# Kernel tuning notes

Measured on AMD Instinct MI355X. Metric: run time of the kernel, lower is better.

Reference implementation:

```python
import jax, jax.numpy as jnp
import numpy as np

N = 100000   # nodes
E = 1000000  # edges
H = 64       # hidden_channels
L = 3        # num_layers
B = 256      # graphs in batch
VOCAB = 100  # embedding table size


def _gru(m, h, wih, whh, bih, bhh):
    # torch.nn.GRUCell semantics, gate order r, z, n
    gi = m @ wih.T + bih            # [N, 3H]
    gh = h @ whh.T + bhh            # [N, 3H]
    ir, iz, inn = jnp.split(gi, 3, axis=-1)
    hr, hz, hn = jnp.split(gh, 3, axis=-1)
    r = jax.nn.sigmoid(ir + hr)
    z = jax.nn.sigmoid(iz + hz)
    n = jnp.tanh(inn + r * hn)
    return (1.0 - z) * n + z * h


def setup_inputs() -> dict:
    key = jax.random.key(0)
    ks = jax.random.split(key, 20)
    s = 1.0 / np.sqrt(H)
    inp = {
        "x": jax.random.randint(ks[0], (N, 1), 0, VOCAB),
        "edge_index": jax.random.randint(ks[1], (2, E), 0, N),
        "edge_attr": jax.random.uniform(ks[2], (E, 1), dtype=jnp.float32),
        "batch": jnp.sort(jax.random.randint(ks[3], (N,), 0, B)),
        "node_emb": jax.random.normal(ks[4], (VOCAB, H), jnp.float32),
        "edge_W": jax.random.normal(ks[5], (H, 1), jnp.float32) * s,
        "edge_b": jnp.zeros((H,), jnp.float32),
        "ggc_W": jax.random.normal(ks[6], (L, H, H), jnp.float32) * s,
        "gru_wih": jax.random.normal(ks[7], (L, 3 * H, H), jnp.float32) * s,
        "gru_whh": jax.random.normal(ks[8], (L, 3 * H, H), jnp.float32) * s,
        "gru_bih": jnp.zeros((L, 3 * H), jnp.float32),
        "gru_bhh": jnp.zeros((L, 3 * H), jnp.float32),
        "fc1_W": jax.random.normal(ks[9], (H // 2, H), jnp.float32) * s,
        "fc1_b": jnp.zeros((H // 2,), jnp.float32),
        "fc2_W": jax.random.normal(ks[10], (H // 4, H // 2), jnp.float32) * (1.0 / np.sqrt(H // 2)),
        "fc2_b": jnp.zeros((H // 4,), jnp.float32),
        "fc3_W": jax.random.normal(ks[11], (1, H // 4), jnp.float32) * (1.0 / np.sqrt(H // 4)),
        "fc3_b": jnp.zeros((1,), jnp.float32),
    }
    return inp


def reference(x, edge_index, edge_attr, batch, node_emb, edge_W, edge_b,
              ggc_W, gru_wih, gru_whh, gru_bih, gru_bhh,
              fc1_W, fc1_b, fc2_W, fc2_b, fc3_W, fc3_b):
    h = node_emb[x[:, 0]]                       # [N, H] node embedding
    _e = edge_attr @ edge_W.T + edge_b          # computed in original, unused by convs
    src, dst = edge_index[0], edge_index[1]
    for l in range(L):
        m = h @ ggc_W[l]                        # per-node linear transform
        agg = jax.ops.segment_sum(m[src], dst, num_segments=N)  # scatter-add to dst
        h = _gru(agg, h, gru_wih[l], gru_whh[l], gru_bih[l], gru_bhh[l])
        h = jax.nn.relu(h)                      # dropout = identity in eval
    sums = jax.ops.segment_sum(h, batch, num_segments=B)
    counts = jax.ops.segment_sum(jnp.ones((N, 1), h.dtype), batch, num_segments=B)
    pooled = sums / jnp.maximum(counts, 1.0)    # global_mean_pool
    y = jax.nn.relu(pooled @ fc1_W.T + fc1_b)
    y = jax.nn.relu(y @ fc2_W.T + fc2_b)
    y = y @ fc3_W.T + fc3_b
    return y[:, 0]                              # squeeze(-1) -> [B]
```

## Files before the change

kernel.cpp:

```cpp
#include <hip/hip_runtime.h>
#include <cstdint>

using h8v = __attribute__((ext_vector_type(8))) _Float16;
using h4v = __attribute__((ext_vector_type(4))) _Float16;
using f4v = __attribute__((ext_vector_type(4))) float;

__device__ __forceinline__ float sigmoidf_(float x) {
  return 1.0f / (1.0f + __expf(-x));
}
__device__ __forceinline__ float tanhf_(float x) {
  return 2.0f / (1.0f + __expf(-2.0f * x)) - 1.0f;
}

#define BN 256
#define BCAP 4096
#define NBMAX 1024

__global__ __launch_bounds__(256) void k_embed(const int* __restrict__ x,
                                               const float* __restrict__ emb,
                                               _Float16* __restrict__ h16, int N) {
  int idx = blockIdx.x * 256 + threadIdx.x;
  if (idx >= N * 64) return;
  int i = idx >> 6, j = idx & 63;
  h16[idx] = (_Float16)emb[x[i] * 64 + j];
}

__global__ __launch_bounds__(256) void k_hist(const int* __restrict__ dst,
                                              int* __restrict__ hist, int E) {
  __shared__ int lh[NBMAX];
  for (int i = threadIdx.x; i < NBMAX; i += 256) lh[i] = 0;
  __syncthreads();
  for (int e = blockIdx.x * 256 + threadIdx.x; e < E; e += gridDim.x * 256)
    atomicAdd(&lh[dst[e] >> 8], 1);
  __syncthreads();
  for (int i = threadIdx.x; i < NBMAX; i += 256)
    if (lh[i]) atomicAdd(&hist[i], lh[i]);
}

__global__ __launch_bounds__(1024) void k_bscan(const int* __restrict__ hist,
                                                int* __restrict__ bbase,
                                                int* __restrict__ rowp,
                                                int nb, int N, int E) {
  __shared__ int sc[NBMAX];
  int t = threadIdx.x;
  int v = (t < nb) ? hist[t] : 0;
  sc[t] = v;
  __syncthreads();
  for (int off = 1; off < NBMAX; off <<= 1) {
    int xx = (t >= off) ? sc[t - off] : 0;
    __syncthreads();
    sc[t] += xx;
    __syncthreads();
  }
  if (t <= nb) bbase[t] = sc[t] - v;
  if (t == 0) rowp[N] = E;
}

#define EPB 4096
__global__ __launch_bounds__(256) void k_scatter(const int* __restrict__ src,
                                                 const int* __restrict__ dst,
                                                 const int* __restrict__ bbase,
                                                 int* __restrict__ cursor,
                                                 unsigned* __restrict__ ebuf,
                                                 int E, int nb) {
  __shared__ int lh[NBMAX];
  __shared__ int lbase[NBMAX];
  for (int i = threadIdx.x; i < NBMAX; i += 256) lh[i] = 0;
  __syncthreads();
  const int e0 = blockIdx.x * EPB;
  const int e1 = min(e0 + EPB, E);
  for (int e = e0 + threadIdx.x; e < e1; e += 256) atomicAdd(&lh[dst[e] >> 8], 1);
  __syncthreads();
  for (int i = threadIdx.x; i < nb; i += 256) {
    int c = lh[i];
    lbase[i] = c ? (bbase[i] + atomicAdd(&cursor[i], c)) : 0;
    lh[i] = 0;
  }
  __syncthreads();
  for (int e = e0 + threadIdx.x; e < e1; e += 256) {
    int d = dst[e];
    int b = d >> 8;
    int off = atomicAdd(&lh[b], 1);
    ebuf[lbase[b] + off] = ((unsigned)(d & 255) << 20) | (unsigned)src[e];
  }
}

__global__ __launch_bounds__(256) void k_csr(const unsigned* __restrict__ ebuf,
                                             const int* __restrict__ bbase,
                                             int* __restrict__ rowp,
                                             int* __restrict__ ssrc, int N) {
  __shared__ unsigned se[BCAP];
  __shared__ int ss[BCAP];
  __shared__ int cnt[BN], excl[BN], sc[BN];
  const int b = blockIdx.x;
  const int t = threadIdx.x;
  const int nbeg = b * BN;
  const int ebeg = bbase[b];
  int ne = bbase[b + 1] - ebeg;
  if (ne > BCAP) ne = BCAP;
  for (int i = t; i < ne; i += 256) se[i] = ebuf[ebeg + i];
  cnt[t] = 0;
  __syncthreads();
  for (int i = t; i < ne; i += 256) atomicAdd(&cnt[se[i] >> 20], 1);
  __syncthreads();
  int v = cnt[t];
  sc[t] = v;
  __syncthreads();
  for (int off = 1; off < BN; off <<= 1) {
    int xx = (t >= off) ? sc[t - off] : 0;
    __syncthreads();
    sc[t] += xx;
    __syncthreads();
  }
  excl[t] = sc[t] - v;
  if (nbeg + t < N) rowp[nbeg + t] = ebeg + excl[t];
  cnt[t] = 0;
  __syncthreads();
  for (int i = t; i < ne; i += 256) {
    unsigned e = se[i];
    int dL = e >> 20;
    int off = atomicAdd(&cnt[dL], 1);
    ss[excl[dL] + off] = (int)(e & 0xFFFFF);
  }
  __syncthreads();
  for (int i = t; i < ne; i += 256) ssrc[ebeg + i] = ss[i];
}

__global__ __launch_bounds__(256) void k_wpack3(const float* __restrict__ wih_all,
                                                const float* __restrict__ ggc_all,
                                                const float* __restrict__ whh_all,
                                                _Float16* __restrict__ Bp) {
  int l = blockIdx.x >> 4;
  int tid = (blockIdx.x & 15) * 256 + threadIdx.x;
  const float* wih = wih_all + (size_t)l * 192 * 64;
  const float* ggc = ggc_all + (size_t)l * 64 * 64;
  const float* whh = whh_all + (size_t)l * 192 * 64;
  int lane = tid & 63;
  int t = (tid >> 6) & 3;
  int wg = tid >> 8;
  int g = wg & 3, w = wg >> 2;
  int j = 16 * w + (lane & 15);
  int kbase = t * 32 + (lane >> 4) * 8;
  _Float16 hv[8];
#pragma unroll
  for (int i = 0; i < 8; ++i) {
    int k = kbase + i;
    float v = 0.0f;
    if (k < 64) {
      if (g < 3) {
        const float* a = wih + (size_t)(g * 64 + j) * 64;
        const float* bp = ggc + (size_t)k * 64;
        float s = 0.0f;
#pragma unroll
        for (int m = 0; m < 64; ++m) s += a[m] * bp[m];
        v = s;
      }
    } else {
      if (g != 2) {
        int row = (g == 3 ? 2 : g) * 64 + j;
        v = whh[(size_t)row * 64 + (k - 64)];
      }
    }
    hv[i] = (_Float16)v;
  }
  _Float16* o = Bp + (size_t)l * 32768 + (size_t)tid * 8;
#pragma unroll
  for (int i = 0; i < 8; ++i) o[i] = hv[i];
}

__device__ __forceinline__ h8v f32lds_to_h8(const float* __restrict__ p) {
  f4v x0 = *(const f4v*)p;
  f4v x1 = *(const f4v*)(p + 4);
  h8v r;
#pragma unroll
  for (int i = 0; i < 4; ++i) {
    r[i] = (_Float16)x0[i];
    r[4 + i] = (_Float16)x1[i];
  }
  return r;
}

#define FSTRIDE 68
#define HSTRIDE 72

__global__ __launch_bounds__(256, 4) void k_gfu(const _Float16* __restrict__ hin16,
                                                _Float16* __restrict__ hout16,
                                                const int* __restrict__ rowp,
                                                const int* __restrict__ ssrc,
                                                const _Float16* __restrict__ Bp,
                                                const float* __restrict__ bih,
                                                const float* __restrict__ bhh,
                                                const int* __restrict__ batch,
                                                float* __restrict__ psum,
                                                float* __restrict__ pcnt,
                                                int N, int nTiles, int last) {
  __shared__ float aggLds[16 * FSTRIDE];
  __shared__ _Float16 hLds[16 * HSTRIDE];
  __shared__ _Float16 oLds[16 * HSTRIDE];
  const int lane = threadIdx.x & 63;
  const int w = threadIdx.x >> 6;
  const int r15 = lane & 15;
  const int kg8 = (lane >> 4) * 8;
  const int jj = w * 16 + r15;

  const float b_r = bih[jj] + bhh[jj];
  const float b_z = bih[64 + jj] + bhh[64 + jj];
  const float b_i = bih[128 + jj];
  const float b_h = bhh[128 + jj];

  h8v b0[4], b1[4], b2[2], b3[2];
#pragma unroll
  for (int t = 0; t < 4; ++t) {
    b0[t] = *(const h8v*)(Bp + ((size_t)((w * 4 + 0) * 4 + t) * 64 + lane) * 8);
    b1[t] = *(const h8v*)(Bp + ((size_t)((w * 4 + 1) * 4 + t) * 64 + lane) * 8);
  }
#pragma unroll
  for (int t = 0; t < 2; ++t) {
    b2[t] = *(const h8v*)(Bp + ((size_t)((w * 4 + 2) * 4 + t) * 64 + lane) * 8);
    b3[t] = *(const h8v*)(Bp + ((size_t)((w * 4 + 3) * 4 + (2 + t)) * 64 + lane) * 8);
  }

  for (int tile = blockIdx.x; tile < nTiles; tile += gridDim.x) {
    const int n0 = tile * 16;
    __syncthreads();
    {
      const int g = lane >> 4;
      const int node = 4 * w + g;
      const int n = n0 + node;
      const int nc = min(n, N - 1);
      h4v hv = *(const h4v*)(hin16 + (size_t)nc * 64 + 4 * r15);
      f4v a0 = {0, 0, 0, 0}, a1 = {0, 0, 0, 0}, a2 = {0, 0, 0, 0}, a3 = {0, 0, 0, 0};
      if (n < N) {
        int e = rowp[n];
        const int end = rowp[n + 1];
        for (; e + 8 <= end; e += 8) {
          int s0 = ssrc[e], s1 = ssrc[e + 1], s2 = ssrc[e + 2], s3 = ssrc[e + 3];
          int s4 = ssrc[e + 4], s5 = ssrc[e + 5], s6 = ssrc[e + 6], s7 = ssrc[e + 7];
          h4v v0 = *(const h4v*)(hin16 + (size_t)s0 * 64 + 4 * r15);
          h4v v1 = *(const h4v*)(hin16 + (size_t)s1 * 64 + 4 * r15);
          h4v v2 = *(const h4v*)(hin16 + (size_t)s2 * 64 + 4 * r15);
          h4v v3 = *(const h4v*)(hin16 + (size_t)s3 * 64 + 4 * r15);
          h4v v4 = *(const h4v*)(hin16 + (size_t)s4 * 64 + 4 * r15);
          h4v v5 = *(const h4v*)(hin16 + (size_t)s5 * 64 + 4 * r15);
          h4v v6 = *(const h4v*)(hin16 + (size_t)s6 * 64 + 4 * r15);
          h4v v7 = *(const h4v*)(hin16 + (size_t)s7 * 64 + 4 * r15);
          a0 += __builtin_convertvector(v0, f4v);
          a1 += __builtin_convertvector(v1, f4v);
          a2 += __builtin_convertvector(v2, f4v);
          a3 += __builtin_convertvector(v3, f4v);
          a0 += __builtin_convertvector(v4, f4v);
          a1 += __builtin_convertvector(v5, f4v);
          a2 += __builtin_convertvector(v6, f4v);
          a3 += __builtin_convertvector(v7, f4v);
        }
        if (e + 4 <= end) {
          int s0 = ssrc[e], s1 = ssrc[e + 1], s2 = ssrc[e + 2], s3 = ssrc[e + 3];
          a0 += __builtin_convertvector(*(const h4v*)(hin16 + (size_t)s0 * 64 + 4 * r15), f4v);
          a1 += __builtin_convertvector(*(const h4v*)(hin16 + (size_t)s1 * 64 + 4 * r15), f4v);
          a2 += __builtin_convertvector(*(const h4v*)(hin16 + (size_t)s2 * 64 + 4 * r15), f4v);
          a3 += __builtin_convertvector(*(const h4v*)(hin16 + (size_t)s3 * 64 + 4 * r15), f4v);
          e += 4;
        }
        if (e + 2 <= end) {
          int s0 = ssrc[e], s1 = ssrc[e + 1];
          a0 += __builtin_convertvector(*(const h4v*)(hin16 + (size_t)s0 * 64 + 4 * r15), f4v);
          a1 += __builtin_convertvector(*(const h4v*)(hin16 + (size_t)s1 * 64 + 4 * r15), f4v);
          e += 2;
        }
        if (e < end) {
          int s0 = ssrc[e];
          a2 += __builtin_convertvector(*(const h4v*)(hin16 + (size_t)s0 * 64 + 4 * r15), f4v);
        }
      }
      a0 += a1; a2 += a3; a0 += a2;
      *(f4v*)(aggLds + node * FSTRIDE + 4 * r15) = a0;
      *(h4v*)(hLds + node * HSTRIDE + 4 * r15) = hv;
    }
    __syncthreads();

    h8v ah[4];
#pragma unroll
    for (int t = 0; t < 2; ++t)
      ah[t] = f32lds_to_h8(aggLds + r15 * FSTRIDE + t * 32 + kg8);
#pragma unroll
    for (int t = 0; t < 2; ++t)
      ah[2 + t] = *(const h8v*)(hLds + r15 * HSTRIDE + t * 32 + kg8);

    f4v acc0 = {0, 0, 0, 0}, acc1 = {0, 0, 0, 0}, acc2 = {0, 0, 0, 0}, acc3 = {0, 0, 0, 0};
#pragma unroll
    for (int t = 0; t < 4; ++t) {
      acc0 = __builtin_amdgcn_mfma_f32_16x16x32_f16(ah[t], b0[t], acc0, 0, 0, 0);
      acc1 = __builtin_amdgcn_mfma_f32_16x16x32_f16(ah[t], b1[t], acc1, 0, 0, 0);
    }
    acc2 = __builtin_amdgcn_mfma_f32_16x16x32_f16(ah[0], b2[0], acc2, 0, 0, 0);
    acc2 = __builtin_amdgcn_mfma_f32_16x16x32_f16(ah[1], b2[1], acc2, 0, 0, 0);
    acc3 = __builtin_amdgcn_mfma_f32_16x16x32_f16(ah[2], b3[0], acc3, 0, 0, 0);
    acc3 = __builtin_amdgcn_mfma_f32_16x16x32_f16(ah[3], b3[1], acc3, 0, 0, 0);

    const int rb = (lane >> 4) * 4;
#pragma unroll
    for (int q = 0; q < 4; ++q) {
      int row = rb + q;
      float hold = (float)hLds[row * HSTRIDE + jj];
      float r = sigmoidf_(acc0[q] + b_r);
      float z = sigmoidf_(acc1[q] + b_z);
      float nv = tanhf_(acc2[q] + b_i + r * (acc3[q] + b_h));
      float o = (1.0f - z) * nv + z * hold;
      oLds[row * HSTRIDE + jj] = (_Float16)fmaxf(o, 0.0f);
    }
    __syncthreads();

    if (!last) {
      const int node = threadIdx.x >> 4;
      const int ci = (threadIdx.x & 15) * 4;
      const int n = n0 + node;
      if (n < N) {
        h4v o = *(const h4v*)(oLds + node * HSTRIDE + ci);
        *(h4v*)(hout16 + (size_t)n * 64 + ci) = o;
      }
    } else {
      if (threadIdx.x < 64) {
        int curb = batch[n0];
        float acc = 0.0f, ca = 0.0f;
#pragma unroll 1
        for (int i = 0; i < 16; ++i) {
          int n = n0 + i;
          if (n >= N) break;
          int b = batch[n];
          if (b != curb) {
            atomicAdd(&psum[curb * 64 + lane], acc);
            if (lane == 0) atomicAdd(&pcnt[curb], ca);
            acc = 0.0f; ca = 0.0f; curb = b;
          }
          acc += (float)oLds[i * HSTRIDE + lane];
          ca += 1.0f;
        }
        atomicAdd(&psum[curb * 64 + lane], acc);
        if (lane == 0) atomicAdd(&pcnt[curb], ca);
      }
    }
  }
}

__global__ __launch_bounds__(64) void k_head(const float* __restrict__ psum,
                                             const float* __restrict__ pcnt,
                                             const float* __restrict__ fc1W,
                                             const float* __restrict__ fc1b,
                                             const float* __restrict__ fc2W,
                                             const float* __restrict__ fc2b,
                                             const float* __restrict__ fc3W,
                                             const float* __restrict__ fc3b,
                                             float* __restrict__ out) {
  int b = blockIdx.x;
  int j = threadIdx.x;
  float c = fmaxf(pcnt[b], 1.0f);
  float p = psum[b * 64 + j] / c;
  int j1 = j & 31;
  float y1 = fc1b[j1];
#pragma unroll
  for (int k = 0; k < 64; ++k) y1 += fc1W[j1 * 64 + k] * __shfl(p, k, 64);
  y1 = fmaxf(y1, 0.0f);
  int j2 = j & 15;
  float y2 = fc2b[j2];
#pragma unroll
  for (int k = 0; k < 32; ++k) y2 += fc2W[j2 * 32 + k] * __shfl(y1, k, 64);
  y2 = fmaxf(y2, 0.0f);
  float y = 0.0f;
#pragma unroll
  for (int k = 0; k < 16; ++k) y += fc3W[k] * __shfl(y2, k, 64);
  if (j == 0) out[b] = y + fc3b[0];
}

extern "C" void kernel_launch(void* const* d_in, const int* in_sizes, int n_in,
                              void* d_out, int out_size, void* d_ws, size_t ws_size,
                              hipStream_t stream) {
  const int N = in_sizes[0];
  const int E = in_sizes[1] / 2;
  const int B = out_size;

  const int* x = (const int*)d_in[0];
  const int* eidx = (const int*)d_in[1];
  const int* batch = (const int*)d_in[3];
  const float* emb = (const float*)d_in[4];
  const float* ggcW = (const float*)d_in[7];
  const float* wih = (const float*)d_in[8];
  const float* whh = (const float*)d_in[9];
  const float* bih = (const float*)d_in[10];
  const float* bhh = (const float*)d_in[11];
  const float* fc1W = (const float*)d_in[12];
  const float* fc1b = (const float*)d_in[13];
  const float* fc2W = (const float*)d_in[14];
  const float* fc2b = (const float*)d_in[15];
  const float* fc3W = (const float*)d_in[16];
  const float* fc3b = (const float*)d_in[17];
  float* out = (float*)d_out;

  const int* srcp = eidx;
  const int* dstp = eidx + E;
  const int nb = (N + BN - 1) / BN;

  char* ws = (char*)d_ws;
  size_t off = 0;
  auto alloc = [&](size_t bytes) -> void* {
    void* p = ws + off;
    off = (off + bytes + 255) & ~(size_t)255;
    return p;
  };
  _Float16* h16a = (_Float16*)alloc((size_t)N * 64 * 2);
  _Float16* h16b = (_Float16*)alloc((size_t)N * 64 * 2);
  int* rowp = (int*)alloc((size_t)(N + 1) * 4);
  int* ssrc = (int*)alloc((size_t)E * 4);
  unsigned* ebuf = (unsigned*)alloc((size_t)E * 4);
  int* hist = (int*)alloc((size_t)NBMAX * 4);
  int* bbase = (int*)alloc((size_t)(NBMAX + 1) * 4);
  int* cursor = (int*)alloc((size_t)NBMAX * 4);
  _Float16* Bp = (_Float16*)alloc((size_t)3 * 32768 * 2);
  float* pool = (float*)alloc((size_t)(B * 64 + B) * 4);
  float* psum = pool;
  float* pcnt = pool + (size_t)B * 64;

  hipMemsetAsync(hist, 0, (size_t)NBMAX * 4, stream);
  hipMemsetAsync(cursor, 0, (size_t)NBMAX * 4, stream);
  hipMemsetAsync(pool, 0, (size_t)(B * 64 + B) * 4, stream);
  k_embed<<<(N * 64 + 255) / 256, 256, 0, stream>>>(x, emb, h16a, N);
  k_hist<<<512, 256, 0, stream>>>(dstp, hist, E);
  k_bscan<<<1, 1024, 0, stream>>>(hist, bbase, rowp, nb, N, E);
  k_scatter<<<(E + EPB - 1) / EPB, 256, 0, stream>>>(srcp, dstp, bbase, cursor,
                                                     ebuf, E, nb);
  k_csr<<<nb, 256, 0, stream>>>(ebuf, bbase, rowp, ssrc, N);
  k_wpack3<<<48, 256, 0, stream>>>(wih, ggcW, whh, Bp);

  const int nTiles = (N + 15) / 16;
  const int grid = nTiles < 2048 ? nTiles : 2048;
  _Float16* hh[2] = {h16a, h16b};
  for (int l = 0; l < 3; ++l) {
    int a = l & 1, b = 1 - a;
    k_gfu<<<grid, 256, 0, stream>>>(hh[a], hh[b], rowp, ssrc,
                                    Bp + (size_t)l * 32768,
                                    bih + (size_t)l * 192, bhh + (size_t)l * 192,
                                    batch, psum, pcnt, N, nTiles, l == 2 ? 1 : 0);
  }

  k_head<<<B, 64, 0, stream>>>(psum, pcnt, fc1W, fc1b, fc2W, fc2b, fc3W, fc3b, out);
}
```

Measured before the change: 235.2 us.

## Pad CSR rows to multiples of eight with zero-row sentinel to drop gather tails

Each destination row's edge list is padded up to a multiple of 8 with a sentinel index N that points at an all-zero extra row in both feature buffers. Rows get explicit begin/end arrays, and blocks claim padded segments through a global atomic cursor. The gather loop then runs only full 8-wide iterations, with no 4/2/1 tail branches. In exchange, the padding adds about 3.5 extra dummy loads per node on average, plus a larger index array and extra setup work.

Measured after the change: 219.4 us. 1.07x faster.

```diff
diff --git a/kernel.cpp b/kernel.cpp
--- a/kernel.cpp
+++ b/kernel.cpp
@@ -18,11 +18,17 @@
 
 __global__ __launch_bounds__(256) void k_embed(const int* __restrict__ x,
                                                const float* __restrict__ emb,
-                                               _Float16* __restrict__ h16, int N) {
+                                               _Float16* __restrict__ h16a,
+                                               _Float16* __restrict__ h16b, int N) {
   int idx = blockIdx.x * 256 + threadIdx.x;
-  if (idx >= N * 64) return;
+  if (idx >= (N + 1) * 64) return;
   int i = idx >> 6, j = idx & 63;
-  h16[idx] = (_Float16)emb[x[i] * 64 + j];
+  if (i < N) {
+    h16a[idx] = (_Float16)emb[x[i] * 64 + j];
+  } else {
+    h16a[idx] = (_Float16)0.0f;
+    h16b[idx] = (_Float16)0.0f;
+  }
 }
 
 __global__ __launch_bounds__(256) void k_hist(const int* __restrict__ dst,
@@ -38,9 +44,7 @@
 }
 
 __global__ __launch_bounds__(1024) void k_bscan(const int* __restrict__ hist,
-                                                int* __restrict__ bbase,
-                                                int* __restrict__ rowp,
-                                                int nb, int N, int E) {
+                                                int* __restrict__ bbase, int nb) {
   __shared__ int sc[NBMAX];
   int t = threadIdx.x;
   int v = (t < nb) ? hist[t] : 0;
@@ -53,7 +57,6 @@
     __syncthreads();
   }
   if (t <= nb) bbase[t] = sc[t] - v;
-  if (t == 0) rowp[N] = E;
 }
 
 #define EPB 4096
@@ -87,11 +90,14 @@
 
 __global__ __launch_bounds__(256) void k_csr(const unsigned* __restrict__ ebuf,
                                              const int* __restrict__ bbase,
+                                             int* __restrict__ padCur,
                                              int* __restrict__ rowp,
+                                             int* __restrict__ rowe,
                                              int* __restrict__ ssrc, int N) {
   __shared__ unsigned se[BCAP];
   __shared__ int ss[BCAP];
-  __shared__ int cnt[BN], excl[BN], sc[BN];
+  __shared__ int cnt[BN], pex[BN], sc[BN];
+  __shared__ int sbase;
   const int b = blockIdx.x;
   const int t = threadIdx.x;
   const int nbeg = b * BN;
@@ -103,8 +109,9 @@
   __syncthreads();
   for (int i = t; i < ne; i += 256) atomicAdd(&cnt[se[i] >> 20], 1);
   __syncthreads();
-  int v = cnt[t];
-  sc[t] = v;
+  const int c = cnt[t];
+  const int p = (c + 7) & ~7;
+  sc[t] = p;
   __syncthreads();
   for (int off = 1; off < BN; off <<= 1) {
     int xx = (t >= off) ? sc[t - off] : 0;
@@ -112,18 +119,26 @@
     sc[t] += xx;
     __syncthreads();
   }
-  excl[t] = sc[t] - v;
-  if (nbeg + t < N) rowp[nbeg + t] = ebeg + excl[t];
+  const int pexcl = sc[t] - p;
+  const int P = sc[BN - 1];
+  if (t == 0) sbase = atomicAdd(padCur, P);
+  pex[t] = pexcl;
   cnt[t] = 0;
   __syncthreads();
+  const int n = nbeg + t;
+  if (n < N) {
+    rowp[n] = sbase + pexcl;
+    rowe[n] = sbase + pexcl + p;
+  }
+  for (int i = c; i < p; ++i) ss[pexcl + i] = N;
   for (int i = t; i < ne; i += 256) {
     unsigned e = se[i];
     int dL = e >> 20;
     int off = atomicAdd(&cnt[dL], 1);
-    ss[excl[dL] + off] = (int)(e & 0xFFFFF);
-  }
-  __syncthreads();
-  for (int i = t; i < ne; i += 256) ssrc[ebeg + i] = ss[i];
+    ss[pex[dL] + off] = (int)(e & 0xFFFFF);
+  }
+  __syncthreads();
+  for (int i = t; i < P; i += 256) ssrc[sbase + i] = ss[i];
 }
 
 __global__ __launch_bounds__(256) void k_wpack3(const float* __restrict__ wih_all,
@@ -186,6 +201,7 @@
 __global__ __launch_bounds__(256, 4) void k_gfu(const _Float16* __restrict__ hin16,
                                                 _Float16* __restrict__ hout16,
                                                 const int* __restrict__ rowp,
+                                                const int* __restrict__ rowe,
                                                 const int* __restrict__ ssrc,
                                                 const _Float16* __restrict__ Bp,
                                                 const float* __restrict__ bih,
@@ -232,8 +248,8 @@
       f4v a0 = {0, 0, 0, 0}, a1 = {0, 0, 0, 0}, a2 = {0, 0, 0, 0}, a3 = {0, 0, 0, 0};
       if (n < N) {
         int e = rowp[n];
-        const int end = rowp[n + 1];
-        for (; e + 8 <= end; e += 8) {
+        const int end = rowe[n];
+        for (; e < end; e += 8) {
           int s0 = ssrc[e], s1 = ssrc[e + 1], s2 = ssrc[e + 2], s3 = ssrc[e + 3];
           int s4 = ssrc[e + 4], s5 = ssrc[e + 5], s6 = ssrc[e + 6], s7 = ssrc[e + 7];
           h4v v0 = *(const h4v*)(hin16 + (size_t)s0 * 64 + 4 * r15);
@@ -252,24 +268,6 @@
           a1 += __builtin_convertvector(v5, f4v);
           a2 += __builtin_convertvector(v6, f4v);
           a3 += __builtin_convertvector(v7, f4v);
-        }
-        if (e + 4 <= end) {
-          int s0 = ssrc[e], s1 = ssrc[e + 1], s2 = ssrc[e + 2], s3 = ssrc[e + 3];
-          a0 += __builtin_convertvector(*(const h4v*)(hin16 + (size_t)s0 * 64 + 4 * r15), f4v);
-          a1 += __builtin_convertvector(*(const h4v*)(hin16 + (size_t)s1 * 64 + 4 * r15), f4v);
-          a2 += __builtin_convertvector(*(const h4v*)(hin16 + (size_t)s2 * 64 + 4 * r15), f4v);
-          a3 += __builtin_convertvector(*(const h4v*)(hin16 + (size_t)s3 * 64 + 4 * r15), f4v);
-          e += 4;
-        }
-        if (e + 2 <= end) {
-          int s0 = ssrc[e], s1 = ssrc[e + 1];
-          a0 += __builtin_convertvector(*(const h4v*)(hin16 + (size_t)s0 * 64 + 4 * r15), f4v);
-          a1 += __builtin_convertvector(*(const h4v*)(hin16 + (size_t)s1 * 64 + 4 * r15), f4v);
-          e += 2;
-        }
-        if (e < end) {
-          int s0 = ssrc[e];
-          a2 += __builtin_convertvector(*(const h4v*)(hin16 + (size_t)s0 * 64 + 4 * r15), f4v);
         }
       }
       a0 += a1; a2 += a3; a0 += a2;
@@ -406,14 +404,16 @@
     off = (off + bytes + 255) & ~(size_t)255;
     return p;
   };
-  _Float16* h16a = (_Float16*)alloc((size_t)N * 64 * 2);
-  _Float16* h16b = (_Float16*)alloc((size_t)N * 64 * 2);
+  _Float16* h16a = (_Float16*)alloc((size_t)(N + 1) * 64 * 2);
+  _Float16* h16b = (_Float16*)alloc((size_t)(N + 1) * 64 * 2);
   int* rowp = (int*)alloc((size_t)(N + 1) * 4);
-  int* ssrc = (int*)alloc((size_t)E * 4);
+  int* rowe = (int*)alloc((size_t)(N + 1) * 4);
+  int* ssrc = (int*)alloc(((size_t)E + 8 * (size_t)N) * 4);
   unsigned* ebuf = (unsigned*)alloc((size_t)E * 4);
   int* hist = (int*)alloc((size_t)NBMAX * 4);
   int* bbase = (int*)alloc((size_t)(NBMAX + 1) * 4);
   int* cursor = (int*)alloc((size_t)NBMAX * 4);
+  int* padCur = (int*)alloc(256);
   _Float16* Bp = (_Float16*)alloc((size_t)3 * 32768 * 2);
   float* pool = (float*)alloc((size_t)(B * 64 + B) * 4);
   float* psum = pool;
@@ -421,13 +421,14 @@
 
   hipMemsetAsync(hist, 0, (size_t)NBMAX * 4, stream);
   hipMemsetAsync(cursor, 0, (size_t)NBMAX * 4, stream);
+  hipMemsetAsync(padCur, 0, 256, stream);
   hipMemsetAsync(pool, 0, (size_t)(B * 64 + B) * 4, stream);
-  k_embed<<<(N * 64 + 255) / 256, 256, 0, stream>>>(x, emb, h16a, N);
+  k_embed<<<((N + 1) * 64 + 255) / 256, 256, 0, stream>>>(x, emb, h16a, h16b, N);
   k_hist<<<512, 256, 0, stream>>>(dstp, hist, E);
-  k_bscan<<<1, 1024, 0, stream>>>(hist, bbase, rowp, nb, N, E);
+  k_bscan<<<1, 1024, 0, stream>>>(hist, bbase, nb);
   k_scatter<<<(E + EPB - 1) / EPB, 256, 0, stream>>>(srcp, dstp, bbase, cursor,
                                                      ebuf, E, nb);
-  k_csr<<<nb, 256, 0, stream>>>(ebuf, bbase, rowp, ssrc, N);
+  k_csr<<<nb, 256, 0, stream>>>(ebuf, bbase, padCur, rowp, rowe, ssrc, N);
   k_wpack3<<<48, 256, 0, stream>>>(wih, ggcW, whh, Bp);
 
   const int nTiles = (N + 15) / 16;
@@ -435,7 +436,7 @@
   _Float16* hh[2] = {h16a, h16b};
   for (int l = 0; l < 3; ++l) {
     int a = l & 1, b = 1 - a;
-    k_gfu<<<grid, 256, 0, stream>>>(hh[a], hh[b], rowp, ssrc,
+    k_gfu<<<grid, 256, 0, stream>>>(hh[a], hh[b], rowp, rowe, ssrc,
                                     Bp + (size_t)l * 32768,
                                     bih + (size_t)l * 192, bhh + (size_t)l * 192,
                                     batch, psum, pcnt, N, nTiles, l == 2 ? 1 : 0);
```
